# Performance work log

Hardware: AMD Instinct MI355X
Metric: run time of the kernel (lower is better)

## Reference

```python
import jax, jax.numpy as jnp
import numpy as np

B, S, D = 2, 2048, 1024
NUM_HEADS = 16
HEAD_DIM = D // NUM_HEADS


def setup_inputs() -> dict:
    key = jax.random.key(0)
    k1, k2, k3, k4 = jax.random.split(key, 4)
    # Weights stored as [d_in, d_out] so projection is x @ W (torch Linear weight transposed).
    scale = 1.0 / np.sqrt(D)
    return {
        "x": jax.random.normal(k1, (B, S, D), dtype=jnp.float32),
        "W_q": jax.random.normal(k2, (D, D), dtype=jnp.float32) * scale,
        "W_k": jax.random.normal(k3, (D, D), dtype=jnp.float32) * scale,
        "W_v": jax.random.normal(k4, (D, D), dtype=jnp.float32) * scale,
    }


def reference(x, W_q, W_k, W_v):
    b, s, d = x.shape
    hd = d // NUM_HEADS
    # QKV projections (no bias, qkv_bias=False)
    q = (x @ W_q).reshape(b, s, NUM_HEADS, hd).transpose(0, 2, 1, 3)  # [B,H,S,hd]
    k = (x @ W_k).reshape(b, s, NUM_HEADS, hd).transpose(0, 2, 1, 3)
    v = (x @ W_v).reshape(b, s, NUM_HEADS, hd).transpose(0, 2, 1, 3)
    # Scaled scores with causal masking (strict upper triangle masked)
    scores = jnp.einsum("bhqd,bhkd->bhqk", q, k) / jnp.sqrt(jnp.float32(hd))
    causal = jnp.triu(jnp.ones((s, s), dtype=bool), 1)  # True = masked
    scores = jnp.where(causal, -jnp.inf, scores)
    attn = jax.nn.softmax(scores, axis=-1)  # dropout is identity (drop_rate=0.0)
    out = jnp.einsum("bhqk,bhkd->bqhd", attn, v).reshape(b, s, d)
    return out
```

## Files before the change

### kernel.cpp

```cpp
#include <hip/hip_runtime.h>


typedef unsigned short u16;
typedef unsigned int u32;
typedef unsigned long long u64;
typedef __bf16 bf16x8 __attribute__((ext_vector_type(8)));
typedef float f32x4 __attribute__((ext_vector_type(4)));
typedef u16 u16x8 __attribute__((ext_vector_type(8)));

#define NB 2
#define NS 2048
#define ND 1024
#define NH 16
#define HD 64

__device__ __forceinline__ u16 f2bf(float f) {
    unsigned int u = __float_as_uint(f);
    unsigned int r = u + 0x7fffu + ((u >> 16) & 1u);
    return (u16)(r >> 16);
}

__device__ __forceinline__ f32x4 mfma16(bf16x8 a, bf16x8 b, f32x4 c) {
    return __builtin_amdgcn_mfma_f32_16x16x32_bf16(a, b, c, 0, 0, 0);
}

__device__ __forceinline__ void gl_lds16(const void* g, void* l) {
    __builtin_amdgcn_global_load_lds(
        (const __attribute__((address_space(1))) unsigned int*)g,
        (__attribute__((address_space(3))) unsigned int*)l, 16, 0, 0);
}

__device__ __forceinline__ bf16x8 ldsw(const u16* base, int row, int colb) {
    return *(const bf16x8*)((const char*)base + row * 128 +
                            (colb ^ ((row & 7) << 4)));
}

__global__ __launch_bounds__(256) void convx_k(const float* __restrict__ x,
                                               u16* __restrict__ xb) {
    int i = (blockIdx.x * 256 + threadIdx.x) * 8;
    const float4* p = (const float4*)(x + i);
    float4 a = p[0], c = p[1];
    u16x8 r;
    r[0] = f2bf(a.x); r[1] = f2bf(a.y); r[2] = f2bf(a.z); r[3] = f2bf(a.w);
    r[4] = f2bf(c.x); r[5] = f2bf(c.y); r[6] = f2bf(c.z); r[7] = f2bf(c.w);
    *(u16x8*)(xb + i) = r;
}

__global__ __launch_bounds__(256) void convw_k(const float* __restrict__ wq,
                                               const float* __restrict__ wk,
                                               const float* __restrict__ wv,
                                               u16* __restrict__ wt) {
    __shared__ float tile[32][33];
    const int z = blockIdx.z;
    const float* W = (z == 0) ? wq : (z == 1) ? wk : wv;
    const int k0 = blockIdx.x * 32, n0 = blockIdx.y * 32;
    const int tx = threadIdx.x & 31, ty = threadIdx.x >> 5;
#pragma unroll
    for (int rr = 0; rr < 32; rr += 8)
        tile[ty + rr][tx] = W[(size_t)(k0 + ty + rr) * ND + n0 + tx];
    __syncthreads();
    u16* dst = wt + (size_t)z * ND * ND;
#pragma unroll
    for (int rr = 0; rr < 32; rr += 8)
        dst[(size_t)(n0 + ty + rr) * ND + k0 + tx] = f2bf(tile[tx][ty + rr]);
}

__global__ __launch_bounds__(256) void qkv_gemm_k(const u16* __restrict__ xb,
                                                  const u16* __restrict__ wt,
                                                  u16* __restrict__ qh,
                                                  u16* __restrict__ kh,
                                                  u16* __restrict__ vt) {
    __shared__ u16 At[128 * 64];
    __shared__ u16 Bt[3][64 * 64];
    const int m0 = blockIdx.x * 128;
    const int n0 = blockIdx.y * 64;
    const int t = threadIdx.x;
    const int lane = t & 63;
    const int wv = t >> 6;
    const int wm = (wv >> 1) * 64, wn = (wv & 1) * 32;
    const int fr = lane & 15;
    const int ks = lane >> 4;

    f32x4 acc[3][4][2] = {};

    for (int kt = 0; kt < ND; kt += 64) {
#pragma unroll
        for (int c = 0; c < 4; c++) {
            const int L = c * 4096 + t * 16;
            const int row = L >> 7;
            const int cb = (L & 127) ^ ((row & 7) << 4);
            gl_lds16((const char*)xb + (size_t)(m0 + row) * 2048 + kt * 2 + cb,
                     (char*)At + L);
        }
#pragma unroll
        for (int z = 0; z < 3; z++)
#pragma unroll
            for (int c = 0; c < 2; c++) {
                const int L = c * 4096 + t * 16;
                const int row = L >> 7;
                const int cb = (L & 127) ^ ((row & 7) << 4);
                gl_lds16((const char*)wt + (size_t)z * (ND * ND * 2) +
                             (size_t)(n0 + row) * 2048 + kt * 2 + cb,
                         (char*)&Bt[z][0] + L);
            }
        __syncthreads();

        bf16x8 fa[4][2];
#pragma unroll
        for (int i = 0; i < 4; i++)
#pragma unroll
            for (int c = 0; c < 2; c++)
                fa[i][c] = ldsw(At, wm + i * 16 + fr, c * 64 + ks * 16);

#pragma unroll
        for (int z = 0; z < 3; z++) {
            bf16x8 fb[2][2];
#pragma unroll
            for (int j = 0; j < 2; j++)
#pragma unroll
                for (int c = 0; c < 2; c++)
                    fb[j][c] =
                        ldsw(&Bt[z][0], wn + j * 16 + fr, c * 64 + ks * 16);
            if (z < 2) {
#pragma unroll
                for (int i = 0; i < 4; i++)
#pragma unroll
                    for (int j = 0; j < 2; j++)
#pragma unroll
                        for (int c = 0; c < 2; c++)
                            acc[z][i][j] =
                                mfma16(fa[i][c], fb[j][c], acc[z][i][j]);
            } else {
#pragma unroll
                for (int i = 0; i < 4; i++)
#pragma unroll
                    for (int j = 0; j < 2; j++)
#pragma unroll
                        for (int c = 0; c < 2; c++)
                            acc[z][i][j] =
                                mfma16(fb[j][c], fa[i][c], acc[z][i][j]);
            }
        }
        __syncthreads();
    }

#pragma unroll
    for (int z = 0; z < 2; z++) {
        u16* dst = (z == 0) ? qh : kh;
#pragma unroll
        for (int i = 0; i < 4; i++)
#pragma unroll
            for (int j = 0; j < 2; j++)
#pragma unroll
                for (int r = 0; r < 4; r++) {
                    int mg = m0 + wm + i * 16 + ks * 4 + r;
                    int ng = n0 + wn + j * 16 + fr;
                    int b = mg >> 11, s = mg & 2047;
                    int hh = ng >> 6, dd = ng & 63;
                    dst[(((size_t)b * NH + hh) * NS + s) * HD + dd] =
                        f2bf(acc[z][i][j][r]);
                }
    }
#pragma unroll
    for (int i = 0; i < 4; i++)
#pragma unroll
        for (int j = 0; j < 2; j++)
#pragma unroll
            for (int r = 0; r < 4; r++) {
                int ng = n0 + wn + j * 16 + ks * 4 + r;
                int mg = m0 + wm + i * 16 + fr;
                int b = mg >> 11, s = mg & 2047;
                int hh = ng >> 6, dd = ng & 63;
                vt[(((size_t)b * NH + hh) * HD + dd) * NS + s] =
                    f2bf(acc[2][i][j][r]);
            }
}


__device__ __forceinline__ void stage_kv(const u16* __restrict__ K,
                                         const u16* __restrict__ V, int kv0,
                                         u16* Kl, u16* Vl, int t) {
#pragma unroll
    for (int c = 0; c < 2; c++) {
        const int L = c * 4096 + t * 16;
        const int row = L >> 7;
        const int cb = (L & 127) ^ ((row & 7) << 4);
        gl_lds16((const char*)K + (size_t)(kv0 + row) * 128 + cb,
                 (char*)Kl + L);
        gl_lds16((const char*)V + (size_t)row * (NS * 2) + kv0 * 2 + cb,
                 (char*)Vl + L);
    }
}

template <bool MASKED>
__device__ __forceinline__ void sm_pxT(const f32x4* sc, u16* pl, int kv0,
                                       int q0, int fr, int ks) {
    const int qg = q0 + fr;
#pragma unroll
    for (int kf = 0; kf < 4; kf++) {
        const int kvb = kv0 + kf * 16 + ks * 4;
        float p[4];
#pragma unroll
        for (int r = 0; r < 4; r++) {
            float s = sc[kf][r];
            if (MASKED && (kvb + r > qg)) s = -3.0e38f;
            p[r] = __expf(fmaf(s, 0.125f, -8.0f));
        }
        u64 w = (u64)f2bf(p[0]) | ((u64)f2bf(p[1]) << 16) |
                ((u64)f2bf(p[2]) << 32) | ((u64)f2bf(p[3]) << 48);
        const int chunk = (2 * kf + (ks >> 1)) ^ (fr & 7);
        *(u64*)((char*)pl + fr * 128 + (chunk << 4) + ((ks & 1) << 3)) = w;
    }
}

__device__ __forceinline__ void pv_lds(const bf16x8 (*fv)[2], const u16* pl,
                                       f32x4* o, f32x4& lacc, bf16x8 ones,
                                       int fr, int ks) {
    bf16x8 pa[2];
#pragma unroll
    for (int s2 = 0; s2 < 2; s2++) {
        const int c = (s2 * 4 + ks) ^ (fr & 7);
        pa[s2] = *(const bf16x8*)((const char*)pl + fr * 128 + (c << 4));
    }
    lacc = mfma16(pa[0], ones, lacc);
    lacc = mfma16(pa[1], ones, lacc);
#pragma unroll
    for (int j = 0; j < 4; j++)
#pragma unroll
        for (int s2 = 0; s2 < 2; s2++) o[j] = mfma16(pa[s2], fv[j][s2], o[j]);
}

__global__ __launch_bounds__(256, 2) void attn_k(const u16* __restrict__ qh,
                                                 const u16* __restrict__ kh,
                                                 const u16* __restrict__ vt,
                                                 float* __restrict__ out) {
    const int t = threadIdx.x, lane = t & 63, wv = t >> 6;
    const int fr = lane & 15, ks = lane >> 4;
    const int bh = blockIdx.x & 31;
    const int p = blockIdx.x >> 5;
    const int b = bh >> 4, h = bh & 15;
    const int tileA = 31 - p, tileB = p;
    const int qA = tileA * 64 + wv * 16;
    const int qB = tileB * 64 + wv * 16;
    const int nA = tileA + 1, nB = tileB + 1;
    const u16* Q = qh + (size_t)bh * NS * HD;
    const u16* K = kh + (size_t)bh * NS * HD;
    const u16* V = vt + (size_t)bh * HD * NS;

    __shared__ u16 Kl[2][64 * 64];
    __shared__ u16 Vl[2][64 * 64];
    __shared__ u16 P[4][2][16 * 64];
    u16* plA = &P[wv][0][0];
    u16* plB = &P[wv][1][0];

    bf16x8 fqA[2], fqB[2];
#pragma unroll
    for (int sl = 0; sl < 2; sl++) {
        fqA[sl] = *(const bf16x8*)&Q[(qA + fr) * HD + sl * 32 + ks * 8];
        fqB[sl] = *(const bf16x8*)&Q[(qB + fr) * HD + sl * 32 + ks * 8];
    }

    u16x8 ob;
#pragma unroll
    for (int j = 0; j < 8; j++) ob[j] = 0x3F80;
    const bf16x8 ones = __builtin_bit_cast(bf16x8, ob);

    f32x4 oA[4] = {}, oB[4] = {};
    f32x4 lA = {}, lB = {};

    stage_kv(K, V, 0, &Kl[0][0], &Vl[0][0], t);
    __syncthreads();

    for (int it = 0; it < nA; ++it) {
        const int cur = it & 1;
        const int kv0 = it * 64;
        if (it + 1 < nA)
            stage_kv(K, V, kv0 + 64, &Kl[cur ^ 1][0], &Vl[cur ^ 1][0], t);

        bf16x8 fk[4][2];
#pragma unroll
        for (int kf = 0; kf < 4; kf++)
#pragma unroll
            for (int sl = 0; sl < 2; sl++)
                fk[kf][sl] = *(const bf16x8*)((const char*)&Kl[cur][0] +
                                              (kf * 16 + fr) * 128 +
                                              ((sl * 64 + ks * 16) ^
                                               ((fr & 7) << 4)));

        f32x4 scA[4] = {};
#pragma unroll
        for (int kf = 0; kf < 4; kf++) {
            scA[kf] = mfma16(fk[kf][0], fqA[0], scA[kf]);
            scA[kf] = mfma16(fk[kf][1], fqA[1], scA[kf]);
        }
        const bool doB = it < nB;
        f32x4 scB[4] = {};
        if (doB) {
#pragma unroll
            for (int kf = 0; kf < 4; kf++) {
                scB[kf] = mfma16(fk[kf][0], fqB[0], scB[kf]);
                scB[kf] = mfma16(fk[kf][1], fqB[1], scB[kf]);
            }
        }

        if (it == nA - 1)
            sm_pxT<true>(scA, plA, kv0, qA, fr, ks);
        else
            sm_pxT<false>(scA, plA, kv0, qA, fr, ks);
        if (doB) {
            if (it == nB - 1)
                sm_pxT<true>(scB, plB, kv0, qB, fr, ks);
            else
                sm_pxT<false>(scB, plB, kv0, qB, fr, ks);
        }

        bf16x8 fv[4][2];
#pragma unroll
        for (int j = 0; j < 4; j++)
#pragma unroll
            for (int s2 = 0; s2 < 2; s2++)
                fv[j][s2] = *(const bf16x8*)((const char*)&Vl[cur][0] +
                                             (j * 16 + fr) * 128 +
                                             ((s2 * 64 + ks * 16) ^
                                              ((fr & 7) << 4)));

        pv_lds(fv, plA, oA, lA, ones, fr, ks);
        if (doB) pv_lds(fv, plB, oB, lB, ones, fr, ks);

        __syncthreads();
    }

    float rlA[4], rlB[4];
#pragma unroll
    for (int r = 0; r < 4; r++) {
        rlA[r] = 1.0f / lA[r];
        rlB[r] = 1.0f / lB[r];
    }
#pragma unroll
    for (int j = 0; j < 4; j++)
#pragma unroll
        for (int r = 0; r < 4; r++) {
            const int qgA = qA + ks * 4 + r;
            const int qgB = qB + ks * 4 + r;
            out[((size_t)b * NS + qgA) * ND + h * HD + j * 16 + fr] =
                oA[j][r] * rlA[r];
            out[((size_t)b * NS + qgB) * ND + h * HD + j * 16 + fr] =
                oB[j][r] * rlB[r];
        }
}

extern "C" void kernel_launch(void* const* d_in, const int* in_sizes, int n_in,
                              void* d_out, int out_size, void* d_ws,
                              size_t ws_size, hipStream_t stream) {
    const float* x = (const float*)d_in[0];
    const float* wq = (const float*)d_in[1];
    const float* wk = (const float*)d_in[2];
    const float* wvp = (const float*)d_in[3];
    float* out = (float*)d_out;

    char* w8 = (char*)d_ws;
    u16* xb = (u16*)(w8);
    u16* wt = (u16*)(w8 + ((size_t)8 << 20));
    u16* qh = (u16*)(w8 + ((size_t)14 << 20));
    u16* kh = (u16*)(w8 + ((size_t)22 << 20));
    u16* vt = (u16*)(w8 + ((size_t)30 << 20));

    convx_k<<<(NB * NS * ND) / (256 * 8), 256, 0, stream>>>(x, xb);
    convw_k<<<dim3(ND / 32, ND / 32, 3), 256, 0, stream>>>(wq, wk, wvp, wt);
    qkv_gemm_k<<<dim3((NB * NS) / 128, ND / 64), 256, 0, stream>>>(
        xb, wt, qh, kh, vt);
    attn_k<<<512, 256, 0, stream>>>(qh, kh, vt, out);
}
```

Before: 81.37 us.

## Give each attention wave 32 query rows and drop paired-tile causal balancing

```diff
diff --git a/kernel.cpp b/kernel.cpp
--- a/kernel.cpp
+++ b/kernel.cpp
@@ -2,9 +2,9 @@
 
 
 typedef unsigned short u16;
-typedef unsigned int u32;
 typedef unsigned long long u64;
 typedef __bf16 bf16x8 __attribute__((ext_vector_type(8)));
+typedef __bf16 bf16x4 __attribute__((ext_vector_type(4)));
 typedef float f32x4 __attribute__((ext_vector_type(4)));
 typedef u16 u16x8 __attribute__((ext_vector_type(8)));
 
@@ -181,8 +181,8 @@
                                          const u16* __restrict__ V, int kv0,
                                          u16* Kl, u16* Vl, int t) {
 #pragma unroll
-    for (int c = 0; c < 2; c++) {
-        const int L = c * 4096 + t * 16;
+    for (int c = 0; c < 4; c++) {
+        const int L = c * 2048 + t * 16;
         const int row = L >> 7;
         const int cb = (L & 127) ^ ((row & 7) << 4);
         gl_lds16((const char*)K + (size_t)(kv0 + row) * 128 + cb,
@@ -193,88 +193,73 @@
 }
 
 template <bool MASKED>
-__device__ __forceinline__ void sm_pxT(const f32x4* sc, u16* pl, int kv0,
+__device__ __forceinline__ void sm_pxT(const f32x4 sc[4][2], u16* pl, int kv0,
                                        int q0, int fr, int ks) {
-    const int qg = q0 + fr;
-#pragma unroll
-    for (int kf = 0; kf < 4; kf++) {
-        const int kvb = kv0 + kf * 16 + ks * 4;
-        float p[4];
-#pragma unroll
-        for (int r = 0; r < 4; r++) {
-            float s = sc[kf][r];
-            if (MASKED && (kvb + r > qg)) s = -3.0e38f;
-            p[r] = __expf(fmaf(s, 0.125f, -8.0f));
+#pragma unroll
+    for (int qf = 0; qf < 2; qf++) {
+        const int row = qf * 16 + fr;
+        const int qg = q0 + row;
+#pragma unroll
+        for (int kf = 0; kf < 4; kf++) {
+            const int kvb = kv0 + kf * 16 + ks * 4;
+            bf16x4 pb;
+#pragma unroll
+            for (int r = 0; r < 4; r++) {
+                float s = sc[kf][qf][r];
+                if (MASKED && (kvb + r > qg)) s = -3.0e38f;
+                pb[r] = (__bf16)__expf(fmaf(s, 0.125f, -8.0f));
+            }
+            const u64 w = __builtin_bit_cast(u64, pb);
+            const int chunk = (2 * kf + (ks >> 1)) ^ (row & 7);
+            *(u64*)((char*)pl + row * 128 + (chunk << 4) + ((ks & 1) << 3)) =
+                w;
         }
-        u64 w = (u64)f2bf(p[0]) | ((u64)f2bf(p[1]) << 16) |
-                ((u64)f2bf(p[2]) << 32) | ((u64)f2bf(p[3]) << 48);
-        const int chunk = (2 * kf + (ks >> 1)) ^ (fr & 7);
-        *(u64*)((char*)pl + fr * 128 + (chunk << 4) + ((ks & 1) << 3)) = w;
-    }
-}
-
-__device__ __forceinline__ void pv_lds(const bf16x8 (*fv)[2], const u16* pl,
-                                       f32x4* o, f32x4& lacc, bf16x8 ones,
-                                       int fr, int ks) {
-    bf16x8 pa[2];
-#pragma unroll
-    for (int s2 = 0; s2 < 2; s2++) {
-        const int c = (s2 * 4 + ks) ^ (fr & 7);
-        pa[s2] = *(const bf16x8*)((const char*)pl + fr * 128 + (c << 4));
-    }
-    lacc = mfma16(pa[0], ones, lacc);
-    lacc = mfma16(pa[1], ones, lacc);
-#pragma unroll
-    for (int j = 0; j < 4; j++)
-#pragma unroll
-        for (int s2 = 0; s2 < 2; s2++) o[j] = mfma16(pa[s2], fv[j][s2], o[j]);
-}
-
-__global__ __launch_bounds__(256, 2) void attn_k(const u16* __restrict__ qh,
+    }
+}
+
+__global__ __launch_bounds__(128, 2) void attn_k(const u16* __restrict__ qh,
                                                  const u16* __restrict__ kh,
                                                  const u16* __restrict__ vt,
                                                  float* __restrict__ out) {
     const int t = threadIdx.x, lane = t & 63, wv = t >> 6;
     const int fr = lane & 15, ks = lane >> 4;
     const int bh = blockIdx.x & 31;
-    const int p = blockIdx.x >> 5;
+    const int tile = 31 - (int)(blockIdx.x >> 5);
     const int b = bh >> 4, h = bh & 15;
-    const int tileA = 31 - p, tileB = p;
-    const int qA = tileA * 64 + wv * 16;
-    const int qB = tileB * 64 + wv * 16;
-    const int nA = tileA + 1, nB = tileB + 1;
+    const int q0 = tile * 64 + wv * 32;
+    const int nIt = tile + 1;
     const u16* Q = qh + (size_t)bh * NS * HD;
     const u16* K = kh + (size_t)bh * NS * HD;
     const u16* V = vt + (size_t)bh * HD * NS;
 
     __shared__ u16 Kl[2][64 * 64];
     __shared__ u16 Vl[2][64 * 64];
-    __shared__ u16 P[4][2][16 * 64];
-    u16* plA = &P[wv][0][0];
-    u16* plB = &P[wv][1][0];
-
-    bf16x8 fqA[2], fqB[2];
-#pragma unroll
-    for (int sl = 0; sl < 2; sl++) {
-        fqA[sl] = *(const bf16x8*)&Q[(qA + fr) * HD + sl * 32 + ks * 8];
-        fqB[sl] = *(const bf16x8*)&Q[(qB + fr) * HD + sl * 32 + ks * 8];
-    }
+    __shared__ u16 P[2][32 * 64];
+    u16* pl = &P[wv][0];
+
+    bf16x8 fq[2][2];
+#pragma unroll
+    for (int qf = 0; qf < 2; qf++)
+#pragma unroll
+        for (int sl = 0; sl < 2; sl++)
+            fq[qf][sl] = *(const bf16x8*)&Q[(q0 + qf * 16 + fr) * HD +
+                                            sl * 32 + ks * 8];
 
     u16x8 ob;
 #pragma unroll
     for (int j = 0; j < 8; j++) ob[j] = 0x3F80;
     const bf16x8 ones = __builtin_bit_cast(bf16x8, ob);
 
-    f32x4 oA[4] = {}, oB[4] = {};
-    f32x4 lA = {}, lB = {};
+    f32x4 o[2][4] = {};
+    f32x4 l[2] = {};
 
     stage_kv(K, V, 0, &Kl[0][0], &Vl[0][0], t);
     __syncthreads();
 
-    for (int it = 0; it < nA; ++it) {
+    for (int it = 0; it < nIt; ++it) {
         const int cur = it & 1;
         const int kv0 = it * 64;
-        if (it + 1 < nA)
+        if (it + 1 < nIt)
             stage_kv(K, V, kv0 + 64, &Kl[cur ^ 1][0], &Vl[cur ^ 1][0], t);
 
         bf16x8 fk[4][2];
@@ -282,71 +267,67 @@
         for (int kf = 0; kf < 4; kf++)
 #pragma unroll
             for (int sl = 0; sl < 2; sl++)
-                fk[kf][sl] = *(const bf16x8*)((const char*)&Kl[cur][0] +
-                                              (kf * 16 + fr) * 128 +
-                                              ((sl * 64 + ks * 16) ^
-                                               ((fr & 7) << 4)));
-
-        f32x4 scA[4] = {};
-#pragma unroll
-        for (int kf = 0; kf < 4; kf++) {
-            scA[kf] = mfma16(fk[kf][0], fqA[0], scA[kf]);
-            scA[kf] = mfma16(fk[kf][1], fqA[1], scA[kf]);
+                fk[kf][sl] = ldsw(&Kl[cur][0], kf * 16 + fr,
+                                  sl * 64 + ks * 16);
+
+        f32x4 sc[4][2] = {};
+#pragma unroll
+        for (int kf = 0; kf < 4; kf++)
+#pragma unroll
+            for (int qf = 0; qf < 2; qf++) {
+                sc[kf][qf] = mfma16(fk[kf][0], fq[qf][0], sc[kf][qf]);
+                sc[kf][qf] = mfma16(fk[kf][1], fq[qf][1], sc[kf][qf]);
+            }
+
+        if (it == nIt - 1)
+            sm_pxT<true>(sc, pl, kv0, q0, fr, ks);
+        else
+            sm_pxT<false>(sc, pl, kv0, q0, fr, ks);
+
+        bf16x8 fv[4][2];
+#pragma unroll
+        for (int j = 0; j < 4; j++)
+#pragma unroll
+            for (int s2 = 0; s2 < 2; s2++)
+                fv[j][s2] = ldsw(&Vl[cur][0], j * 16 + fr,
+                                 s2 * 64 + ks * 16);
+
+#pragma unroll
+        for (int qf = 0; qf < 2; qf++) {
+            bf16x8 pa[2];
+#pragma unroll
+            for (int s2 = 0; s2 < 2; s2++) {
+                const int row = qf * 16 + fr;
+                const int c = (s2 * 4 + ks) ^ (row & 7);
+                pa[s2] =
+                    *(const bf16x8*)((const char*)pl + row * 128 + (c << 4));
+            }
+            l[qf] = mfma16(pa[0], ones, l[qf]);
+            l[qf] = mfma16(pa[1], ones, l[qf]);
+#pragma unroll
+            for (int j = 0; j < 4; j++)
+#pragma unroll
+                for (int s2 = 0; s2 < 2; s2++)
+                    o[qf][j] = mfma16(pa[s2], fv[j][s2], o[qf][j]);
         }
-        const bool doB = it < nB;
-        f32x4 scB[4] = {};
-        if (doB) {
-#pragma unroll
-            for (int kf = 0; kf < 4; kf++) {
-                scB[kf] = mfma16(fk[kf][0], fqB[0], scB[kf]);
-                scB[kf] = mfma16(fk[kf][1], fqB[1], scB[kf]);
-            }
-        }
-
-        if (it == nA - 1)
-            sm_pxT<true>(scA, plA, kv0, qA, fr, ks);
-        else
-            sm_pxT<false>(scA, plA, kv0, qA, fr, ks);
-        if (doB) {
-            if (it == nB - 1)
-                sm_pxT<true>(scB, plB, kv0, qB, fr, ks);
-            else
-                sm_pxT<false>(scB, plB, kv0, qB, fr, ks);
-        }
-
-        bf16x8 fv[4][2];
+
+        __syncthreads();
+    }
+
+#pragma unroll
+    for (int qf = 0; qf < 2; qf++) {
+        float rl[4];
+#pragma unroll
+        for (int r = 0; r < 4; r++) rl[r] = 1.0f / l[qf][r];
 #pragma unroll
         for (int j = 0; j < 4; j++)
 #pragma unroll
-            for (int s2 = 0; s2 < 2; s2++)
-                fv[j][s2] = *(const bf16x8*)((const char*)&Vl[cur][0] +
-                                             (j * 16 + fr) * 128 +
-                                             ((s2 * 64 + ks * 16) ^
-                                              ((fr & 7) << 4)));
-
-        pv_lds(fv, plA, oA, lA, ones, fr, ks);
-        if (doB) pv_lds(fv, plB, oB, lB, ones, fr, ks);
-
-        __syncthreads();
-    }
-
-    float rlA[4], rlB[4];
-#pragma unroll
-    for (int r = 0; r < 4; r++) {
-        rlA[r] = 1.0f / lA[r];
-        rlB[r] = 1.0f / lB[r];
-    }
-#pragma unroll
-    for (int j = 0; j < 4; j++)
-#pragma unroll
-        for (int r = 0; r < 4; r++) {
-            const int qgA = qA + ks * 4 + r;
-            const int qgB = qB + ks * 4 + r;
-            out[((size_t)b * NS + qgA) * ND + h * HD + j * 16 + fr] =
-                oA[j][r] * rlA[r];
-            out[((size_t)b * NS + qgB) * ND + h * HD + j * 16 + fr] =
-                oB[j][r] * rlB[r];
-        }
+            for (int r = 0; r < 4; r++) {
+                const int qg = q0 + qf * 16 + ks * 4 + r;
+                out[((size_t)b * NS + qg) * ND + h * HD + j * 16 + fr] =
+                    o[qf][j][r] * rl[r];
+            }
+    }
 }
 
 extern "C" void kernel_launch(void* const* d_in, const int* in_sizes, int n_in,
@@ -369,5 +350,5 @@
     convw_k<<<dim3(ND / 32, ND / 32, 3), 256, 0, stream>>>(wq, wk, wvp, wt);
     qkv_gemm_k<<<dim3((NB * NS) / 128, ND / 64), 256, 0, stream>>>(
         xb, wt, qh, kh, vt);
-    attn_k<<<512, 256, 0, stream>>>(qh, kh, vt, out);
-}
+    attn_k<<<1024, 128, 0, stream>>>(qh, kh, vt, out);
+}
```

Result: slower. 85.77 us (+5.4%).

## Load V fragments directly from global memory and raise MFMA wave priority

Applied to the files above, without the earlier changes.

```diff
diff --git a/kernel.cpp b/kernel.cpp
--- a/kernel.cpp
+++ b/kernel.cpp
@@ -2,7 +2,6 @@
 
 
 typedef unsigned short u16;
-typedef unsigned int u32;
 typedef unsigned long long u64;
 typedef __bf16 bf16x8 __attribute__((ext_vector_type(8)));
 typedef float f32x4 __attribute__((ext_vector_type(4)));
@@ -177,9 +176,8 @@
 }
 
 
-__device__ __forceinline__ void stage_kv(const u16* __restrict__ K,
-                                         const u16* __restrict__ V, int kv0,
-                                         u16* Kl, u16* Vl, int t) {
+__device__ __forceinline__ void stage_k(const u16* __restrict__ K, int kv0,
+                                        u16* Kl, int t) {
 #pragma unroll
     for (int c = 0; c < 2; c++) {
         const int L = c * 4096 + t * 16;
@@ -187,8 +185,6 @@
         const int cb = (L & 127) ^ ((row & 7) << 4);
         gl_lds16((const char*)K + (size_t)(kv0 + row) * 128 + cb,
                  (char*)Kl + L);
-        gl_lds16((const char*)V + (size_t)row * (NS * 2) + kv0 * 2 + cb,
-                 (char*)Vl + L);
     }
 }
 
@@ -213,21 +209,23 @@
     }
 }
 
-__device__ __forceinline__ void pv_lds(const bf16x8 (*fv)[2], const u16* pl,
-                                       f32x4* o, f32x4& lacc, bf16x8 ones,
-                                       int fr, int ks) {
+__device__ __forceinline__ void pv_g(const bf16x8 (*fv)[2], const u16* pl,
+                                     f32x4* o, f32x4& lacc, bf16x8 ones,
+                                     int fr, int ks) {
     bf16x8 pa[2];
 #pragma unroll
     for (int s2 = 0; s2 < 2; s2++) {
         const int c = (s2 * 4 + ks) ^ (fr & 7);
         pa[s2] = *(const bf16x8*)((const char*)pl + fr * 128 + (c << 4));
     }
+    __builtin_amdgcn_s_setprio(1);
     lacc = mfma16(pa[0], ones, lacc);
     lacc = mfma16(pa[1], ones, lacc);
 #pragma unroll
     for (int j = 0; j < 4; j++)
 #pragma unroll
         for (int s2 = 0; s2 < 2; s2++) o[j] = mfma16(pa[s2], fv[j][s2], o[j]);
+    __builtin_amdgcn_s_setprio(0);
 }
 
 __global__ __launch_bounds__(256, 2) void attn_k(const u16* __restrict__ qh,
@@ -248,7 +246,6 @@
     const u16* V = vt + (size_t)bh * HD * NS;
 
     __shared__ u16 Kl[2][64 * 64];
-    __shared__ u16 Vl[2][64 * 64];
     __shared__ u16 P[4][2][16 * 64];
     u16* plA = &P[wv][0][0];
     u16* plB = &P[wv][1][0];
@@ -268,33 +265,38 @@
     f32x4 oA[4] = {}, oB[4] = {};
     f32x4 lA = {}, lB = {};
 
-    stage_kv(K, V, 0, &Kl[0][0], &Vl[0][0], t);
+    stage_k(K, 0, &Kl[0][0], t);
     __syncthreads();
 
     for (int it = 0; it < nA; ++it) {
         const int cur = it & 1;
         const int kv0 = it * 64;
-        if (it + 1 < nA)
-            stage_kv(K, V, kv0 + 64, &Kl[cur ^ 1][0], &Vl[cur ^ 1][0], t);
+        if (it + 1 < nA) stage_k(K, kv0 + 64, &Kl[cur ^ 1][0], t);
 
         bf16x8 fk[4][2];
 #pragma unroll
         for (int kf = 0; kf < 4; kf++)
 #pragma unroll
             for (int sl = 0; sl < 2; sl++)
-                fk[kf][sl] = *(const bf16x8*)((const char*)&Kl[cur][0] +
-                                              (kf * 16 + fr) * 128 +
-                                              ((sl * 64 + ks * 16) ^
-                                               ((fr & 7) << 4)));
-
-        f32x4 scA[4] = {};
+                fk[kf][sl] = ldsw(&Kl[cur][0], kf * 16 + fr,
+                                  sl * 64 + ks * 16);
+
+        bf16x8 fv[4][2];
+#pragma unroll
+        for (int j = 0; j < 4; j++)
+#pragma unroll
+            for (int s2 = 0; s2 < 2; s2++)
+                fv[j][s2] = *(const bf16x8*)&V[(j * 16 + fr) * NS + kv0 +
+                                               s2 * 32 + ks * 8];
+
+        f32x4 scA[4] = {}, scB[4] = {};
+        const bool doB = it < nB;
+        __builtin_amdgcn_s_setprio(1);
 #pragma unroll
         for (int kf = 0; kf < 4; kf++) {
             scA[kf] = mfma16(fk[kf][0], fqA[0], scA[kf]);
             scA[kf] = mfma16(fk[kf][1], fqA[1], scA[kf]);
         }
-        const bool doB = it < nB;
-        f32x4 scB[4] = {};
         if (doB) {
 #pragma unroll
             for (int kf = 0; kf < 4; kf++) {
@@ -302,6 +304,7 @@
                 scB[kf] = mfma16(fk[kf][1], fqB[1], scB[kf]);
             }
         }
+        __builtin_amdgcn_s_setprio(0);
 
         if (it == nA - 1)
             sm_pxT<true>(scA, plA, kv0, qA, fr, ks);
@@ -314,18 +317,8 @@
                 sm_pxT<false>(scB, plB, kv0, qB, fr, ks);
         }
 
-        bf16x8 fv[4][2];
-#pragma unroll
-        for (int j = 0; j < 4; j++)
-#pragma unroll
-            for (int s2 = 0; s2 < 2; s2++)
-                fv[j][s2] = *(const bf16x8*)((const char*)&Vl[cur][0] +
-                                             (j * 16 + fr) * 128 +
-                                             ((s2 * 64 + ks * 16) ^
-                                              ((fr & 7) << 4)));
-
-        pv_lds(fv, plA, oA, lA, ones, fr, ks);
-        if (doB) pv_lds(fv, plB, oB, lB, ones, fr, ks);
+        pv_g(fv, plA, oA, lA, ones, fr, ks);
+        if (doB) pv_g(fv, plB, oB, lB, ones, fr, ks);
 
         __syncthreads();
     }
```

Result: slower. 108.6 us (+33.5%).

## Keep softmax probabilities in registers by permuting V^T layout; drop P LDS round-trip

Applied to the files above, without the earlier changes.

```diff
diff --git a/kernel.cpp b/kernel.cpp
--- a/kernel.cpp
+++ b/kernel.cpp
@@ -2,7 +2,6 @@
 
 
 typedef unsigned short u16;
-typedef unsigned int u32;
 typedef unsigned long long u64;
 typedef __bf16 bf16x8 __attribute__((ext_vector_type(8)));
 typedef float f32x4 __attribute__((ext_vector_type(4)));
@@ -171,7 +170,10 @@
                 int mg = m0 + wm + i * 16 + fr;
                 int b = mg >> 11, s = mg & 2047;
                 int hh = ng >> 6, dd = ng & 63;
-                vt[(((size_t)b * NH + hh) * HD + dd) * NS + s] =
+                int w = s & 63;
+                int sp = (s & ~63) | (w & 32) | (((w >> 2) & 3) << 3) |
+                         (((w >> 4) & 1) << 2) | (w & 3);
+                vt[(((size_t)b * NH + hh) * HD + dd) * NS + sp] =
                     f2bf(acc[2][i][j][r]);
             }
 }
@@ -193,41 +195,31 @@
 }
 
 template <bool MASKED>
-__device__ __forceinline__ void sm_pxT(const f32x4* sc, u16* pl, int kv0,
-                                       int q0, int fr, int ks) {
+__device__ __forceinline__ void sm_pack(const f32x4* sc, bf16x8 pa[2],
+                                        int kv0, int q0, int fr, int ks) {
     const int qg = q0 + fr;
 #pragma unroll
-    for (int kf = 0; kf < 4; kf++) {
-        const int kvb = kv0 + kf * 16 + ks * 4;
-        float p[4];
+    for (int kf = 0; kf < 4; kf++)
 #pragma unroll
         for (int r = 0; r < 4; r++) {
             float s = sc[kf][r];
-            if (MASKED && (kvb + r > qg)) s = -3.0e38f;
-            p[r] = __expf(fmaf(s, 0.125f, -8.0f));
-        }
-        u64 w = (u64)f2bf(p[0]) | ((u64)f2bf(p[1]) << 16) |
-                ((u64)f2bf(p[2]) << 32) | ((u64)f2bf(p[3]) << 48);
-        const int chunk = (2 * kf + (ks >> 1)) ^ (fr & 7);
-        *(u64*)((char*)pl + fr * 128 + (chunk << 4) + ((ks & 1) << 3)) = w;
-    }
-}
-
-__device__ __forceinline__ void pv_lds(const bf16x8 (*fv)[2], const u16* pl,
-                                       f32x4* o, f32x4& lacc, bf16x8 ones,
-                                       int fr, int ks) {
-    bf16x8 pa[2];
-#pragma unroll
-    for (int s2 = 0; s2 < 2; s2++) {
-        const int c = (s2 * 4 + ks) ^ (fr & 7);
-        pa[s2] = *(const bf16x8*)((const char*)pl + fr * 128 + (c << 4));
-    }
+            if (MASKED && (kv0 + kf * 16 + ks * 4 + r > qg)) s = -3.0e38f;
+            pa[kf >> 1][(kf & 1) * 4 + r] =
+                (__bf16)exp2f(fmaf(s, 0.18033688f, -11.5415603f));
+        }
+}
+
+__device__ __forceinline__ void pv_reg(const bf16x8 (*fv)[2],
+                                       const bf16x8 pa[2], f32x4* o,
+                                       f32x4& lacc, bf16x8 ones) {
+    __builtin_amdgcn_s_setprio(1);
     lacc = mfma16(pa[0], ones, lacc);
     lacc = mfma16(pa[1], ones, lacc);
 #pragma unroll
     for (int j = 0; j < 4; j++)
 #pragma unroll
         for (int s2 = 0; s2 < 2; s2++) o[j] = mfma16(pa[s2], fv[j][s2], o[j]);
+    __builtin_amdgcn_s_setprio(0);
 }
 
 __global__ __launch_bounds__(256, 2) void attn_k(const u16* __restrict__ qh,
@@ -249,9 +241,6 @@
 
     __shared__ u16 Kl[2][64 * 64];
     __shared__ u16 Vl[2][64 * 64];
-    __shared__ u16 P[4][2][16 * 64];
-    u16* plA = &P[wv][0][0];
-    u16* plB = &P[wv][1][0];
 
     bf16x8 fqA[2], fqB[2];
 #pragma unroll
@@ -282,19 +271,17 @@
         for (int kf = 0; kf < 4; kf++)
 #pragma unroll
             for (int sl = 0; sl < 2; sl++)
-                fk[kf][sl] = *(const bf16x8*)((const char*)&Kl[cur][0] +
-                                              (kf * 16 + fr) * 128 +
-                                              ((sl * 64 + ks * 16) ^
-                                               ((fr & 7) << 4)));
-
-        f32x4 scA[4] = {};
+                fk[kf][sl] =
+                    ldsw(&Kl[cur][0], kf * 16 + fr, sl * 64 + ks * 16);
+
+        f32x4 scA[4] = {}, scB[4] = {};
+        const bool doB = it < nB;
+        __builtin_amdgcn_s_setprio(1);
 #pragma unroll
         for (int kf = 0; kf < 4; kf++) {
             scA[kf] = mfma16(fk[kf][0], fqA[0], scA[kf]);
             scA[kf] = mfma16(fk[kf][1], fqA[1], scA[kf]);
         }
-        const bool doB = it < nB;
-        f32x4 scB[4] = {};
         if (doB) {
 #pragma unroll
             for (int kf = 0; kf < 4; kf++) {
@@ -302,30 +289,30 @@
                 scB[kf] = mfma16(fk[kf][1], fqB[1], scB[kf]);
             }
         }
-
+        __builtin_amdgcn_s_setprio(0);
+
+        bf16x8 fv[4][2];
+#pragma unroll
+        for (int j = 0; j < 4; j++)
+#pragma unroll
+            for (int s2 = 0; s2 < 2; s2++)
+                fv[j][s2] =
+                    ldsw(&Vl[cur][0], j * 16 + fr, s2 * 64 + ks * 16);
+
+        bf16x8 paA[2], paB[2];
         if (it == nA - 1)
-            sm_pxT<true>(scA, plA, kv0, qA, fr, ks);
+            sm_pack<true>(scA, paA, kv0, qA, fr, ks);
         else
-            sm_pxT<false>(scA, plA, kv0, qA, fr, ks);
+            sm_pack<false>(scA, paA, kv0, qA, fr, ks);
+        pv_reg(fv, paA, oA, lA, ones);
+
         if (doB) {
             if (it == nB - 1)
-                sm_pxT<true>(scB, plB, kv0, qB, fr, ks);
+                sm_pack<true>(scB, paB, kv0, qB, fr, ks);
             else
-                sm_pxT<false>(scB, plB, kv0, qB, fr, ks);
-        }
-
-        bf16x8 fv[4][2];
-#pragma unroll
-        for (int j = 0; j < 4; j++)
-#pragma unroll
-            for (int s2 = 0; s2 < 2; s2++)
-                fv[j][s2] = *(const bf16x8*)((const char*)&Vl[cur][0] +
-                                             (j * 16 + fr) * 128 +
-                                             ((s2 * 64 + ks * 16) ^
-                                              ((fr & 7) << 4)));
-
-        pv_lds(fv, plA, oA, lA, ones, fr, ks);
-        if (doB) pv_lds(fv, plB, oB, lB, ones, fr, ks);
+                sm_pack<false>(scB, paB, kv0, qB, fr, ks);
+            pv_reg(fv, paB, oB, lB, ones);
+        }
 
         __syncthreads();
     }
```

After: 81.67 us. About the same (+0.4%).
